# Kernel optimization log

Measured on AMD Instinct MI355X. Metric: run time of the kernel, lower is better.

Reference implementation:

```python
import jax, jax.numpy as jnp
import numpy as np

B, S, H, A = 16, 2048, 512, 256


def setup_inputs() -> dict:
    key = jax.random.key(0)
    k1, k2, k3 = jax.random.split(key, 3)
    x = jax.random.normal(k1, (B, S, H), dtype=jnp.float32)
    W_a = jax.random.normal(k2, (A, H), dtype=jnp.float32) * (1.0 / np.sqrt(H))
    q = jax.random.normal(k3, (1, A), dtype=jnp.float32) * (1.0 / np.sqrt(A))
    return {"x": x, "W_a": W_a, "q": q}


def reference(x, W_a, q):
    # x: [B,S,H], W_a: [A,H], q: [1,A]
    Bm, Sm, Hm = x.shape
    # Per-key score e[b,t] = q . tanh(W_a @ x[b,t]).
    # In the original, keys for t > s are zeroed BEFORE the bias-free linear;
    # tanh(0)=0 and the -inf softmax mask removes those entries, so the score
    # is independent of the query position s -> no O(S^2*H*A) recompute needed.
    e = jnp.einsum('oa,bta->bt', q, jnp.tanh(jnp.einsum('bth,ah->bta', x, W_a)))  # [B,S]
    causal = jnp.where(jnp.tril(jnp.ones((Sm, Sm), dtype=bool)), 0.0, -jnp.inf)  # [S_query, S_key]
    logits = e[:, None, :] + causal[None, :, :]            # [B,S,S]
    d = jax.nn.softmax(logits, axis=-1)                    # attention over keys t<=s
    # masked values v_masked[b,s,t,:] = [t<=s]*x[b,t,:]; d is already 0 for t>s
    a = jnp.einsum('bst,bth->bsh', d, x)                   # [B,S,H]
    return a[:, :, None, :], d[:, :, None, :]              # [B,S,1,H], [B,S,1,S] as in torch
```

## Files before the change

### kernel.cpp

```cpp
#include <hip/hip_runtime.h>
#include <hip/hip_bf16.h>
#include <math.h>

#define BB 16
#define SS 2048
#define HH 512
#define AA 256
#define NCH 64
#define CT  (SS/NCH)

__global__ __launch_bounds__(256, 2) void gemm_e_kernel(
    const float* __restrict__ x, const float* __restrict__ W,
    const float* __restrict__ q, float* __restrict__ e)
{
    __shared__ float Wl[64][256];
    __shared__ float Xl[64][64];
    const int tid  = threadIdx.x;
    const int lane = tid & 63;
    const int wv   = tid >> 6;
    const long tok0 = (long)blockIdx.x * 64;

    float acc[4][16];
    #pragma unroll
    for (int i = 0; i < 4; i++)
        #pragma unroll
        for (int j = 0; j < 16; j++) acc[i][j] = 0.f;

    for (int hc = 0; hc < HH; hc += 64) {
        __syncthreads();
        #pragma unroll
        for (int r = 0; r < 16; r++) {
            int idx = r * 256 + tid;
            int a   = idx >> 4;
            int h4  = idx & 15;
            float4 v = *(const float4*)&W[(long)a * HH + hc + h4 * 4];
            int col = (((a >> 2) ^ (h4 & 7)) << 2) + (a & 3);
            int hh = h4 * 4;
            Wl[hh + 0][col] = v.x; Wl[hh + 1][col] = v.y;
            Wl[hh + 2][col] = v.z; Wl[hh + 3][col] = v.w;
        }
        #pragma unroll
        for (int r = 0; r < 4; r++) {
            int idx = r * 256 + tid;
            int t   = idx >> 4;
            int h4  = idx & 15;
            float4 v = *(const float4*)&x[(tok0 + t) * HH + hc + h4 * 4];
            int col = (((t >> 2) ^ (h4 & 7)) << 2) + (t & 3);
            int hh = h4 * 4;
            Xl[hh + 0][col] = v.x; Xl[hh + 1][col] = v.y;
            Xl[hh + 2][col] = v.z; Xl[hh + 3][col] = v.w;
        }
        __syncthreads();
        #pragma unroll 4
        for (int h = 0; h < 64; h++) {
            const int sh = (h >> 2) & 7;
            float4 wvv = *(const float4*)&Wl[h][(lane ^ sh) << 2];
            float xv[16];
            #pragma unroll
            for (int j4 = 0; j4 < 4; j4++) {
                float4 xx = *(const float4*)&Xl[h][(((wv << 2) + j4) ^ sh) << 2];
                xv[j4 * 4 + 0] = xx.x; xv[j4 * 4 + 1] = xx.y;
                xv[j4 * 4 + 2] = xx.z; xv[j4 * 4 + 3] = xx.w;
            }
            #pragma unroll
            for (int j = 0; j < 16; j++) {
                acc[0][j] = fmaf(wvv.x, xv[j], acc[0][j]);
                acc[1][j] = fmaf(wvv.y, xv[j], acc[1][j]);
                acc[2][j] = fmaf(wvv.z, xv[j], acc[2][j]);
                acc[3][j] = fmaf(wvv.w, xv[j], acc[3][j]);
            }
        }
    }
    float4 qv = *(const float4*)&q[lane * 4];
    #pragma unroll
    for (int j = 0; j < 16; j++) {
        float sv = qv.x * tanhf(acc[0][j]) + qv.y * tanhf(acc[1][j])
                 + qv.z * tanhf(acc[2][j]) + qv.w * tanhf(acc[3][j]);
        #pragma unroll
        for (int off = 32; off > 0; off >>= 1) sv += __shfl_xor(sv, off, 64);
        if (lane == 0) e[tok0 + wv * 16 + j] = sv;
    }
}

__global__ __launch_bounds__(256) void softmax_scan_kernel(
    const float* __restrict__ e, float* __restrict__ w, float* __restrict__ zinv)
{
    __shared__ float red[256];
    const int b = blockIdx.x, tid = threadIdx.x;
    const float* eb = e + b * SS;
    float v[8];
    #pragma unroll
    for (int j = 0; j < 8; j++) v[j] = eb[tid * 8 + j];
    float m = v[0];
    #pragma unroll
    for (int j = 1; j < 8; j++) m = fmaxf(m, v[j]);
    red[tid] = m; __syncthreads();
    for (int st = 128; st > 0; st >>= 1) {
        if (tid < st) red[tid] = fmaxf(red[tid], red[tid + st]);
        __syncthreads();
    }
    const float mb = red[0];
    __syncthreads();
    float we[8], pf[8], p = 0.f;
    #pragma unroll
    for (int j = 0; j < 8; j++) { we[j] = expf(v[j] - mb); p += we[j]; pf[j] = p; }
    red[tid] = p; __syncthreads();
    for (int st = 1; st < 256; st <<= 1) {
        float t = (tid >= st) ? red[tid - st] : 0.f;
        __syncthreads();
        red[tid] += t;
        __syncthreads();
    }
    const float excl = red[tid] - p;
    #pragma unroll
    for (int j = 0; j < 8; j++) {
        float Z = excl + pf[j];
        w[b * SS + tid * 8 + j]    = we[j];
        zinv[b * SS + tid * 8 + j] = 1.0f / Z;
    }
}

__global__ __launch_bounds__(256) void write_d_kernel(
    const float* __restrict__ w, const float* __restrict__ zinv,
    float* __restrict__ dout)
{
    const int bs = blockIdx.x;
    const int b  = bs >> 11;
    const int s  = bs & (SS - 1);
    const float zi = zinv[bs];
    const float4* wb = (const float4*)(w + b * SS);
    float4* row = (float4*)(dout + (size_t)bs * SS);
    #pragma unroll
    for (int r = 0; r < 2; r++) {
        int t4 = r * 256 + threadIdx.x;
        int t  = t4 * 4;
        float4 wv = wb[t4];
        float4 o;
        o.x = (t + 0 <= s) ? wv.x * zi : 0.f;
        o.y = (t + 1 <= s) ? wv.y * zi : 0.f;
        o.z = (t + 2 <= s) ? wv.z * zi : 0.f;
        o.w = (t + 3 <= s) ? wv.w * zi : 0.f;
        row[t4] = o;
    }
}

__global__ __launch_bounds__(128) void scan_part_kernel(
    const float* __restrict__ x, const float* __restrict__ w, float* __restrict__ P)
{
    const int blk = blockIdx.x;
    const int b = blk >> 6;
    const int c = blk & 63;
    const int tid = threadIdx.x;
    const int t0 = c * CT;
    const float4* xb = (const float4*)(x + ((size_t)b * SS + t0) * HH);
    const float* wb = w + b * SS + t0;
    float4 acc = make_float4(0.f, 0.f, 0.f, 0.f);
    for (int t = 0; t < CT; t++) {
        float wt = wb[t];
        float4 xv = xb[(size_t)t * (HH / 4) + tid];
        acc.x = fmaf(wt, xv.x, acc.x);
        acc.y = fmaf(wt, xv.y, acc.y);
        acc.z = fmaf(wt, xv.z, acc.z);
        acc.w = fmaf(wt, xv.w, acc.w);
    }
    ((float4*)P)[(size_t)blk * (HH / 4) + tid] = acc;
}

__global__ __launch_bounds__(128) void scan_emit_kernel(
    const float* __restrict__ x, const float* __restrict__ w,
    const float* __restrict__ zinv, const float* __restrict__ P,
    float* __restrict__ aout)
{
    const int blk = blockIdx.x;
    const int b = blk >> 6;
    const int c = blk & 63;
    const int tid = threadIdx.x;
    float4 base = make_float4(0.f, 0.f, 0.f, 0.f);
    for (int cc = 0; cc < c; cc++) {
        float4 p = ((const float4*)P)[(size_t)(b * NCH + cc) * (HH / 4) + tid];
        base.x += p.x; base.y += p.y; base.z += p.z; base.w += p.w;
    }
    const int t0 = c * CT;
    const float4* xb = (const float4*)(x + ((size_t)b * SS + t0) * HH);
    const float* wb = w + b * SS + t0;
    const float* zb = zinv + b * SS + t0;
    float4* ab = (float4*)(aout + ((size_t)b * SS + t0) * HH);
    for (int t = 0; t < CT; t++) {
        float wt = wb[t];
        float zi = zb[t];
        float4 xv = xb[(size_t)t * (HH / 4) + tid];
        base.x = fmaf(wt, xv.x, base.x);
        base.y = fmaf(wt, xv.y, base.y);
        base.z = fmaf(wt, xv.z, base.z);
        base.w = fmaf(wt, xv.w, base.w);
        float4 o = make_float4(base.x * zi, base.y * zi, base.z * zi, base.w * zi);
        ab[(size_t)t * (HH / 4) + tid] = o;
    }
}

extern "C" void kernel_launch(void* const* d_in, const int* in_sizes, int n_in,
                              void* d_out, int out_size, void* d_ws, size_t ws_size,
                              hipStream_t stream)
{
    const float* x = (const float*)d_in[0];
    const float* W = (const float*)d_in[1];
    const float* q = (const float*)d_in[2];
    float* out  = (float*)d_out;
    float* aout = out;
    float* dout = out + (size_t)BB * SS * HH;

    float* ws   = (float*)d_ws;
    float* e    = ws;
    float* w    = ws + BB * SS;
    float* zinv = ws + 2 * BB * SS;
    float* P    = ws + 3 * BB * SS;

    hipLaunchKernelGGL(gemm_e_kernel, dim3(BB * SS / 64), dim3(256), 0, stream,
                       x, W, q, e);
    hipLaunchKernelGGL(softmax_scan_kernel, dim3(BB), dim3(256), 0, stream,
                       e, w, zinv);
    hipLaunchKernelGGL(write_d_kernel, dim3(BB * SS), dim3(256), 0, stream,
                       w, zinv, dout);
    hipLaunchKernelGGL(scan_part_kernel, dim3(BB * NCH), dim3(128), 0, stream,
                       x, w, P);
    hipLaunchKernelGGL(scan_emit_kernel, dim3(BB * NCH), dim3(128), 0, stream,
                       x, w, zinv, P, aout);
}
```

Before: 517.1 us.

## Use bf16 MFMA for score GEMM, add chunk prefix kernel, nontemporal stores

Moves the score GEMM from fp32 FMAs to bf16 MFMA 16x16x32, converting W to bf16 in a separate kernel and x to bf16 while staging it in LDS. It also doubles the number of scan chunks, adds a per-batch prefix kernel so scan_emit no longer re-sums earlier partials, unrolls the scan loops, and uses nontemporal stores for the large d and a outputs. Lower precision in the logits could change the softmax weights a little.

```diff
diff --git a/kernel.cpp b/kernel.cpp
--- a/kernel.cpp
+++ b/kernel.cpp
@@ -6,80 +6,114 @@
 #define SS 2048
 #define HH 512
 #define AA 256
-#define NCH 64
+#define NCH 128
 #define CT  (SS/NCH)
-
-__global__ __launch_bounds__(256, 2) void gemm_e_kernel(
-    const float* __restrict__ x, const float* __restrict__ W,
+#define XST 72
+
+typedef short bf16x8 __attribute__((ext_vector_type(8)));
+typedef float f32x4  __attribute__((ext_vector_type(4)));
+
+__device__ __forceinline__ short f2bf(float f) {
+    union { __hip_bfloat16 h; short s; } u;
+    u.h = __float2bfloat16(f);
+    return u.s;
+}
+
+__device__ __forceinline__ void nt_store4(float4 v, float4* p) {
+    f32x4 o = {v.x, v.y, v.z, v.w};
+    __builtin_nontemporal_store(o, (f32x4*)p);
+}
+
+__global__ __launch_bounds__(256) void convW_kernel(
+    const float* __restrict__ W, short* __restrict__ Wb)
+{
+    int i = blockIdx.x * 256 + threadIdx.x;
+    float4 v = ((const float4*)W)[i];
+    short4 o = make_short4(f2bf(v.x), f2bf(v.y), f2bf(v.z), f2bf(v.w));
+    ((short4*)Wb)[i] = o;
+}
+
+__global__ __launch_bounds__(256, 2) void gemm_e_mfma(
+    const float* __restrict__ x, const short* __restrict__ Wb,
     const float* __restrict__ q, float* __restrict__ e)
 {
-    __shared__ float Wl[64][256];
-    __shared__ float Xl[64][64];
+    __shared__ short Xl[64 * XST];
+    __shared__ short Wl[256 * XST];
+    __shared__ float epart[2][64];
+
     const int tid  = threadIdx.x;
     const int lane = tid & 63;
     const int wv   = tid >> 6;
+    const int wm   = wv & 1;
+    const int wn   = wv >> 1;
+    const int quad = lane >> 4;
+    const int col  = lane & 15;
     const long tok0 = (long)blockIdx.x * 64;
 
-    float acc[4][16];
-    #pragma unroll
-    for (int i = 0; i < 4; i++)
-        #pragma unroll
-        for (int j = 0; j < 16; j++) acc[i][j] = 0.f;
-
-    for (int hc = 0; hc < HH; hc += 64) {
-        __syncthreads();
-        #pragma unroll
-        for (int r = 0; r < 16; r++) {
-            int idx = r * 256 + tid;
-            int a   = idx >> 4;
-            int h4  = idx & 15;
-            float4 v = *(const float4*)&W[(long)a * HH + hc + h4 * 4];
-            int col = (((a >> 2) ^ (h4 & 7)) << 2) + (a & 3);
-            int hh = h4 * 4;
-            Wl[hh + 0][col] = v.x; Wl[hh + 1][col] = v.y;
-            Wl[hh + 2][col] = v.z; Wl[hh + 3][col] = v.w;
-        }
-        #pragma unroll
-        for (int r = 0; r < 4; r++) {
-            int idx = r * 256 + tid;
-            int t   = idx >> 4;
-            int h4  = idx & 15;
-            float4 v = *(const float4*)&x[(tok0 + t) * HH + hc + h4 * 4];
-            int col = (((t >> 2) ^ (h4 & 7)) << 2) + (t & 3);
-            int hh = h4 * 4;
-            Xl[hh + 0][col] = v.x; Xl[hh + 1][col] = v.y;
-            Xl[hh + 2][col] = v.z; Xl[hh + 3][col] = v.w;
-        }
-        __syncthreads();
-        #pragma unroll 4
-        for (int h = 0; h < 64; h++) {
-            const int sh = (h >> 2) & 7;
-            float4 wvv = *(const float4*)&Wl[h][(lane ^ sh) << 2];
-            float xv[16];
-            #pragma unroll
-            for (int j4 = 0; j4 < 4; j4++) {
-                float4 xx = *(const float4*)&Xl[h][(((wv << 2) + j4) ^ sh) << 2];
-                xv[j4 * 4 + 0] = xx.x; xv[j4 * 4 + 1] = xx.y;
-                xv[j4 * 4 + 2] = xx.z; xv[j4 * 4 + 3] = xx.w;
-            }
-            #pragma unroll
-            for (int j = 0; j < 16; j++) {
-                acc[0][j] = fmaf(wvv.x, xv[j], acc[0][j]);
-                acc[1][j] = fmaf(wvv.y, xv[j], acc[1][j]);
-                acc[2][j] = fmaf(wvv.z, xv[j], acc[2][j]);
-                acc[3][j] = fmaf(wvv.w, xv[j], acc[3][j]);
-            }
-        }
-    }
-    float4 qv = *(const float4*)&q[lane * 4];
-    #pragma unroll
-    for (int j = 0; j < 16; j++) {
-        float sv = qv.x * tanhf(acc[0][j]) + qv.y * tanhf(acc[1][j])
-                 + qv.z * tanhf(acc[2][j]) + qv.w * tanhf(acc[3][j]);
-        #pragma unroll
-        for (int off = 32; off > 0; off >>= 1) sv += __shfl_xor(sv, off, 64);
-        if (lane == 0) e[tok0 + wv * 16 + j] = sv;
-    }
+    f32x4 acc[2][8];
+    #pragma unroll
+    for (int mt = 0; mt < 2; mt++)
+        #pragma unroll
+        for (int nt = 0; nt < 8; nt++) acc[mt][nt] = (f32x4){0.f, 0.f, 0.f, 0.f};
+
+    for (int kc = 0; kc < HH; kc += 64) {
+        __syncthreads();
+        #pragma unroll
+        for (int i = 0; i < 2; i++) {
+            int task = i * 256 + tid;
+            int row = task >> 3, seg = task & 7;
+            const float* src = &x[(tok0 + row) * HH + kc + seg * 8];
+            float4 v0 = *(const float4*)src;
+            float4 v1 = *(const float4*)(src + 4);
+            bf16x8 o;
+            o[0] = f2bf(v0.x); o[1] = f2bf(v0.y); o[2] = f2bf(v0.z); o[3] = f2bf(v0.w);
+            o[4] = f2bf(v1.x); o[5] = f2bf(v1.y); o[6] = f2bf(v1.z); o[7] = f2bf(v1.w);
+            *(bf16x8*)&Xl[row * XST + seg * 8] = o;
+        }
+        #pragma unroll
+        for (int i = 0; i < 8; i++) {
+            int task = i * 256 + tid;
+            int row = task >> 3, seg = task & 7;
+            bf16x8 v = *(const bf16x8*)&Wb[row * HH + kc + seg * 8];
+            *(bf16x8*)&Wl[row * XST + seg * 8] = v;
+        }
+        __syncthreads();
+        #pragma unroll
+        for (int kk = 0; kk < 64; kk += 32) {
+            bf16x8 af[2], bfr[8];
+            #pragma unroll
+            for (int mt = 0; mt < 2; mt++)
+                af[mt] = *(bf16x8*)&Xl[(wm * 32 + mt * 16 + col) * XST + kk + quad * 8];
+            #pragma unroll
+            for (int nt = 0; nt < 8; nt++)
+                bfr[nt] = *(bf16x8*)&Wl[(wn * 128 + nt * 16 + col) * XST + kk + quad * 8];
+            #pragma unroll
+            for (int mt = 0; mt < 2; mt++)
+                #pragma unroll
+                for (int nt = 0; nt < 8; nt++)
+                    acc[mt][nt] = __builtin_amdgcn_mfma_f32_16x16x32_bf16(
+                        af[mt], bfr[nt], acc[mt][nt], 0, 0, 0);
+        }
+    }
+
+    float qv[8];
+    #pragma unroll
+    for (int nt = 0; nt < 8; nt++) qv[nt] = q[wn * 128 + nt * 16 + col];
+    #pragma unroll
+    for (int mt = 0; mt < 2; mt++) {
+        #pragma unroll
+        for (int reg = 0; reg < 4; reg++) {
+            float sv = 0.f;
+            #pragma unroll
+            for (int nt = 0; nt < 8; nt++) sv += qv[nt] * tanhf(acc[mt][nt][reg]);
+            #pragma unroll
+            for (int off = 1; off < 16; off <<= 1) sv += __shfl_xor(sv, off, 64);
+            if (col == 0)
+                epart[wn][wm * 32 + mt * 16 + quad * 4 + reg] = sv;
+        }
+    }
+    __syncthreads();
+    if (tid < 64) e[tok0 + tid] = epart[0][tid] + epart[1][tid];
 }
 
 __global__ __launch_bounds__(256) void softmax_scan_kernel(
@@ -140,7 +174,7 @@
         o.y = (t + 1 <= s) ? wv.y * zi : 0.f;
         o.z = (t + 2 <= s) ? wv.z * zi : 0.f;
         o.w = (t + 3 <= s) ? wv.w * zi : 0.f;
-        row[t4] = o;
+        nt_store4(o, &row[t4]);
     }
 }
 
@@ -148,13 +182,14 @@
     const float* __restrict__ x, const float* __restrict__ w, float* __restrict__ P)
 {
     const int blk = blockIdx.x;
-    const int b = blk >> 6;
-    const int c = blk & 63;
+    const int b = blk >> 7;
+    const int c = blk & (NCH - 1);
     const int tid = threadIdx.x;
     const int t0 = c * CT;
     const float4* xb = (const float4*)(x + ((size_t)b * SS + t0) * HH);
     const float* wb = w + b * SS + t0;
     float4 acc = make_float4(0.f, 0.f, 0.f, 0.f);
+    #pragma unroll 4
     for (int t = 0; t < CT; t++) {
         float wt = wb[t];
         float4 xv = xb[(size_t)t * (HH / 4) + tid];
@@ -166,25 +201,43 @@
     ((float4*)P)[(size_t)blk * (HH / 4) + tid] = acc;
 }
 
+__global__ __launch_bounds__(128) void chunk_prefix_kernel(float* __restrict__ P)
+{
+    const int b = blockIdx.x, tid = threadIdx.x;
+    float4* Pb = (float4*)P + (size_t)b * NCH * (HH / 4) + tid;
+    float4 run = make_float4(0.f, 0.f, 0.f, 0.f);
+    for (int c = 0; c < NCH; c += 4) {
+        float4 p0 = Pb[(size_t)(c + 0) * (HH / 4)];
+        float4 p1 = Pb[(size_t)(c + 1) * (HH / 4)];
+        float4 p2 = Pb[(size_t)(c + 2) * (HH / 4)];
+        float4 p3 = Pb[(size_t)(c + 3) * (HH / 4)];
+        Pb[(size_t)(c + 0) * (HH / 4)] = run;
+        run.x += p0.x; run.y += p0.y; run.z += p0.z; run.w += p0.w;
+        Pb[(size_t)(c + 1) * (HH / 4)] = run;
+        run.x += p1.x; run.y += p1.y; run.z += p1.z; run.w += p1.w;
+        Pb[(size_t)(c + 2) * (HH / 4)] = run;
+        run.x += p2.x; run.y += p2.y; run.z += p2.z; run.w += p2.w;
+        Pb[(size_t)(c + 3) * (HH / 4)] = run;
+        run.x += p3.x; run.y += p3.y; run.z += p3.z; run.w += p3.w;
+    }
+}
+
 __global__ __launch_bounds__(128) void scan_emit_kernel(
     const float* __restrict__ x, const float* __restrict__ w,
     const float* __restrict__ zinv, const float* __restrict__ P,
     float* __restrict__ aout)
 {
     const int blk = blockIdx.x;
-    const int b = blk >> 6;
-    const int c = blk & 63;
+    const int b = blk >> 7;
+    const int c = blk & (NCH - 1);
     const int tid = threadIdx.x;
-    float4 base = make_float4(0.f, 0.f, 0.f, 0.f);
-    for (int cc = 0; cc < c; cc++) {
-        float4 p = ((const float4*)P)[(size_t)(b * NCH + cc) * (HH / 4) + tid];
-        base.x += p.x; base.y += p.y; base.z += p.z; base.w += p.w;
-    }
+    float4 base = ((const float4*)P)[(size_t)blk * (HH / 4) + tid];
     const int t0 = c * CT;
     const float4* xb = (const float4*)(x + ((size_t)b * SS + t0) * HH);
     const float* wb = w + b * SS + t0;
     const float* zb = zinv + b * SS + t0;
     float4* ab = (float4*)(aout + ((size_t)b * SS + t0) * HH);
+    #pragma unroll 4
     for (int t = 0; t < CT; t++) {
         float wt = wb[t];
         float zi = zb[t];
@@ -194,7 +247,7 @@
         base.z = fmaf(wt, xv.z, base.z);
         base.w = fmaf(wt, xv.w, base.w);
         float4 o = make_float4(base.x * zi, base.y * zi, base.z * zi, base.w * zi);
-        ab[(size_t)t * (HH / 4) + tid] = o;
+        nt_store4(o, &ab[(size_t)t * (HH / 4) + tid]);
     }
 }
 
@@ -214,15 +267,20 @@
     float* w    = ws + BB * SS;
     float* zinv = ws + 2 * BB * SS;
     float* P    = ws + 3 * BB * SS;
-
-    hipLaunchKernelGGL(gemm_e_kernel, dim3(BB * SS / 64), dim3(256), 0, stream,
-                       x, W, q, e);
+    short* Wb   = (short*)(ws + 3 * BB * SS + BB * NCH * HH);
+
+    hipLaunchKernelGGL(convW_kernel, dim3(AA * HH / 4 / 256), dim3(256), 0, stream,
+                       W, Wb);
+    hipLaunchKernelGGL(gemm_e_mfma, dim3(BB * SS / 64), dim3(256), 0, stream,
+                       x, Wb, q, e);
     hipLaunchKernelGGL(softmax_scan_kernel, dim3(BB), dim3(256), 0, stream,
                        e, w, zinv);
     hipLaunchKernelGGL(write_d_kernel, dim3(BB * SS), dim3(256), 0, stream,
                        w, zinv, dout);
     hipLaunchKernelGGL(scan_part_kernel, dim3(BB * NCH), dim3(128), 0, stream,
                        x, w, P);
+    hipLaunchKernelGGL(chunk_prefix_kernel, dim3(BB), dim3(128), 0, stream,
+                       P);
     hipLaunchKernelGGL(scan_emit_kernel, dim3(BB * NCH), dim3(128), 0, stream,
                        x, w, zinv, P, aout);
 }
```

After: 433.0 us. 16.3% less time.
